# Kernel optimization log

Measured on AMD Instinct MI355X. Metric: run time of the kernel, lower is better.

Reference implementation:

```python
import jax, jax.numpy as jnp
import numpy as np


def setup_inputs() -> dict:
    key = jax.random.key(0)
    k1, k2 = jax.random.split(key)
    B, D, T = 8, 256, 4096
    Q, K = 8, 1024
    z = jax.random.normal(k1, (B, D, T), dtype=jnp.float32)
    # original init: uniform(-1/n_e, 1/n_e)
    codebooks = jax.random.uniform(k2, (Q, K, D), dtype=jnp.float32,
                                   minval=-1.0 / K, maxval=1.0 / K)
    return {"z": z, "codebooks": codebooks}


def reference(z, codebooks):
    # z: [B, e_dim, T]; codebooks: [Q, n_e, e_dim]
    zp = jnp.transpose(z, (0, 2, 1))  # [B, T, D]
    residual = zp
    quantized_out = jnp.zeros_like(zp)
    total_loss = jnp.zeros((), dtype=z.dtype)
    all_indices = []
    Q = codebooks.shape[0]
    for q in range(Q):  # small fixed number of residual stages
        E = codebooks[q]  # [K, D]
        # squared euclidean distances: ||r||^2 + ||e||^2 - 2 r.e
        d = (jnp.sum(residual ** 2, axis=-1, keepdims=True)
             + jnp.sum(E ** 2, axis=-1)
             - 2.0 * jnp.einsum('btd,kd->btk', residual, E))  # [B, T, K]
        idx = jnp.argmin(d, axis=-1)  # [B, T]
        z_q = E[idx]                  # [B, T, D] gather
        loss = (jnp.mean((jax.lax.stop_gradient(z_q) - residual) ** 2)
                + 0.25 * jnp.mean((z_q - jax.lax.stop_gradient(residual)) ** 2))
        # straight-through estimator
        z_q_st = residual + jax.lax.stop_gradient(z_q - residual)
        residual = residual - z_q_st
        quantized_out = quantized_out + z_q_st
        total_loss = total_loss + loss
        all_indices.append(idx)
    quantized_out = jnp.transpose(quantized_out, (0, 2, 1))  # [B, D, T]
    return quantized_out, total_loss, jnp.stack(all_indices)  # indices: [Q, B, T]
```

## Files before the change

### kernel.cpp

```cpp
#include <hip/hip_runtime.h>

#define B_   8
#define D_   256
#define T_   4096
#define Q_   8
#define K_   1024
#define BT_  (B_*T_)
#define N_   (B_*T_*D_)
#define LOSS_OFF N_
#define IDX_OFF  (N_+1)
#define ROWS 64
#define THREADS 1024

typedef __attribute__((ext_vector_type(8))) short short8;
typedef __attribute__((ext_vector_type(4))) float float4v;

union U4S8 { uint4 u; short8 s; };

__device__ __forceinline__ unsigned short f2bf(float x) {
    unsigned int u = __float_as_uint(x);
    unsigned int r = (u + 0x7FFFu + ((u >> 16) & 1u)) >> 16;
    return (unsigned short)r;
}
__device__ __forceinline__ float bf2f(unsigned short b) {
    return __uint_as_float(((unsigned int)b) << 16);
}
__device__ __forceinline__ unsigned fkey(float f) {
    unsigned u = __float_as_uint(f);
    return (u & 0x80000000u) ? ~u : (u | 0x80000000u);
}
__device__ __forceinline__ float fkeyinv(unsigned k) {
    unsigned u = (k & 0x80000000u) ? (k & 0x7fffffffu) : ~k;
    return __uint_as_float(u);
}


__global__ void k_init(const float* __restrict__ z, float* __restrict__ residual,
                       double* lossAcc) {
    __shared__ float tile[32][33];
    int b  = blockIdx.z;
    int d0 = blockIdx.y * 32;
    int t0 = blockIdx.x * 32;
    int tx = threadIdx.x & 31;
    int ty = threadIdx.x >> 5;
    const float* zb = z + (size_t)b * D_ * T_;
    #pragma unroll
    for (int r = 0; r < 32; r += 8)
        tile[ty + r][tx] = zb[(size_t)(d0 + ty + r) * T_ + t0 + tx];
    __syncthreads();
    float* rb = residual + (size_t)b * T_ * D_;
    #pragma unroll
    for (int r = 0; r < 32; r += 8)
        rb[(size_t)(t0 + ty + r) * D_ + d0 + tx] = tile[tx][ty + r];
    if (b == 0 && blockIdx.x == 0 && blockIdx.y == 0 && threadIdx.x == 0)
        *lossAcc = 0.0;
}


__global__ void k_bfrag(const float* __restrict__ cb, uint4* __restrict__ Bfrag) {
    int gid = blockIdx.x * 256 + threadIdx.x;
    int q    = gid >> 15;
    int rem  = gid & 32767;
    int ct   = rem >> 9;
    int kc   = (rem >> 6) & 7;
    int lane = rem & 63;
    int cand = ct * 16 + (lane & 15);
    int kb   = kc * 32 + (lane >> 4) * 8;
    const float* e = cb + ((size_t)q * K_ + cand) * D_ + kb;
    float4v u0 = *(const float4v*)(e);
    float4v u1 = *(const float4v*)(e + 4);
    float vv[8] = {u0.x, u0.y, u0.z, u0.w, u1.x, u1.y, u1.z, u1.w};
    unsigned short h[8], l[8];
    #pragma unroll
    for (int j = 0; j < 8; ++j) {
        float v = vv[j];
        h[j] = f2bf(v);
        l[j] = f2bf(v - bf2f(h[j]));
    }
    uint4 hi, lo;
    hi.x = (unsigned)h[0] | ((unsigned)h[1] << 16);
    hi.y = (unsigned)h[2] | ((unsigned)h[3] << 16);
    hi.z = (unsigned)h[4] | ((unsigned)h[5] << 16);
    hi.w = (unsigned)h[6] | ((unsigned)h[7] << 16);
    lo.x = (unsigned)l[0] | ((unsigned)l[1] << 16);
    lo.y = (unsigned)l[2] | ((unsigned)l[3] << 16);
    lo.z = (unsigned)l[4] | ((unsigned)l[5] << 16);
    lo.w = (unsigned)l[6] | ((unsigned)l[7] << 16);
    size_t base = (((size_t)(q * 64 + ct) * 8 + kc) * 2) * 64;
    Bfrag[base + lane]      = hi;
    Bfrag[base + 64 + lane] = lo;
}


__global__ void k_se(const float* __restrict__ cb, float* __restrict__ Se) {
    int gid = blockIdx.x * 256 + threadIdx.x;
    int i  = gid >> 4;
    int ln = gid & 15;
    if (i >= Q_ * K_) return;
    const float* e = cb + (size_t)i * D_ + ln * 16;
    float4v v0 = *(const float4v*)(e);
    float4v v1 = *(const float4v*)(e + 4);
    float4v v2 = *(const float4v*)(e + 8);
    float4v v3 = *(const float4v*)(e + 12);
    float vv[16] = {v0.x, v0.y, v0.z, v0.w, v1.x, v1.y, v1.z, v1.w,
                    v2.x, v2.y, v2.z, v2.w, v3.x, v3.y, v3.z, v3.w};
    double s = 0.0;
    #pragma unroll
    for (int d = 0; d < 16; ++d) {
        float a = vv[d] * vv[d];
        s += (double)a;
    }
    #pragma unroll
    for (int st = 8; st > 0; st >>= 1) s += __shfl_xor(s, st);
    if (ln == 0) Se[i] = (float)s;
}


__launch_bounds__(THREADS, 1)
__global__ void k_stage(const float* __restrict__ cb,
                        const uint4* __restrict__ Bfrag,
                        const float* __restrict__ Se,
                        float* __restrict__ residual,
                        float* __restrict__ out,
                        double* __restrict__ lossAcc,
                        int q) {
    __shared__ union {
        uint4 afr[4096];
        struct { int slist[64][16]; float sdd[64][16];
                 int srow[1024]; int sslot[1024]; } post;
        struct { float ovd[1024]; int ovk[1024]; } over;
        double lred[16];
    } sc;
    __shared__ float seL[1024];
    __shared__ float srb[64], margin[64];
    __shared__ unsigned sminI[64];
    __shared__ int   scount[64], sidx[64];
    __shared__ int   nSurv;

    const int tid  = threadIdx.x;
    const int lane = tid & 63;
    const int w    = tid >> 6;
    const int quad = lane >> 4;
    const int lc   = lane & 15;
    const int row0 = blockIdx.x * ROWS;
    const int g    = tid >> 8;
    const int dt   = tid & 255;

    if (tid < 64) { scount[tid] = 0; sminI[tid] = 0xFFFFFFFFu; }
    if (tid == 64) nSurv = 0;
    seL[tid] = Se[q * K_ + tid];

    const uint4* __restrict__ Bq = Bfrag + (size_t)q * (64 * 8 * 2 * 64);
    U4S8 bh0[2], bl0[2], bh1[2], bl1[2];
    #pragma unroll
    for (int c = 0; c < 2; ++c) {
        const uint4* p0 = Bq + (((size_t)((w * 4 + c) * 8 + 0)) * 2) * 64 + lane;
        bh0[c].u = p0[0]; bl0[c].u = p0[64];
        const uint4* p1 = Bq + (((size_t)((w * 4 + 2 + c) * 8 + 0)) * 2) * 64 + lane;
        bh1[c].u = p1[0]; bl1[c].u = p1[64];
    }

    {
        int row = tid >> 4, seg = tid & 15;
        int rg = row >> 4, rlo = row & 15;
        int kc = seg >> 1, par = seg & 1;
        const float* rp = residual + (size_t)(row0 + row) * D_ + seg * 16;
        float4v v0 = *(const float4v*)(rp);
        float4v v1 = *(const float4v*)(rp + 4);
        float4v v2 = *(const float4v*)(rp + 8);
        float4v v3 = *(const float4v*)(rp + 12);
        float vv[16] = {v0.x, v0.y, v0.z, v0.w, v1.x, v1.y, v1.z, v1.w,
                        v2.x, v2.y, v2.z, v2.w, v3.x, v3.y, v3.z, v3.w};
        double s = 0.0; float sa = 0.0f;
        #pragma unroll
        for (int i = 0; i < 16; ++i) {
            float v = vv[i];
            s += (double)(v * v);
            sa += fabsf(v);
        }
        #pragma unroll
        for (int st = 8; st > 0; st >>= 1) {
            s  += __shfl_xor(s, st);
            sa += __shfl_xor(sa, st);
        }
        if (seg == 0) {
            float sr = (float)s;
            float sb = sa * 1.001f;
            srb[row]    = sr;
            margin[row] = 9.6e-7f * sr + 4.0e-7f * sb + 2.0e-4f;
        }
        #pragma unroll
        for (int h = 0; h < 2; ++h) {
            unsigned short hh[8], ll[8];
            #pragma unroll
            for (int j = 0; j < 8; ++j) {
                float v = vv[h * 8 + j];
                hh[j] = f2bf(v);
                ll[j] = f2bf(v - bf2f(hh[j]));
            }
            uint4 hiW, loW;
            hiW.x = (unsigned)hh[0] | ((unsigned)hh[1] << 16);
            hiW.y = (unsigned)hh[2] | ((unsigned)hh[3] << 16);
            hiW.z = (unsigned)hh[4] | ((unsigned)hh[5] << 16);
            hiW.w = (unsigned)hh[6] | ((unsigned)hh[7] << 16);
            loW.x = (unsigned)ll[0] | ((unsigned)ll[1] << 16);
            loW.y = (unsigned)ll[2] | ((unsigned)ll[3] << 16);
            loW.z = (unsigned)ll[4] | ((unsigned)ll[5] << 16);
            loW.w = (unsigned)ll[6] | ((unsigned)ll[7] << 16);
            int ln = (par * 2 + h) * 16 + rlo;
            int sl = ln ^ kc;
            sc.afr[((rg * 8 + kc) * 2 + 0) * 64 + sl] = hiW;
            sc.afr[((rg * 8 + kc) * 2 + 1) * 64 + sl] = loW;
        }
    }
    __syncthreads();

    float4v accA[16];
    #pragma unroll
    for (int i = 0; i < 16; ++i) accA[i] = (float4v){0.f, 0.f, 0.f, 0.f};

    for (int s = 0; s < 16; ++s) {
        int kc = s >> 1;
        int cb0 = (s & 1) * 2;
        U4S8 bh[2], bl[2];
        if ((s & 1) == 0) { bh[0] = bh0[0]; bl[0] = bl0[0]; bh[1] = bh0[1]; bl[1] = bl0[1]; }
        else              { bh[0] = bh1[0]; bl[0] = bl1[0]; bh[1] = bh1[1]; bl[1] = bl1[1]; }
        {
            int ps  = (s + 2 > 15) ? 15 : (s + 2);
            int pkc = ps >> 1;
            int pc0 = (ps & 1) * 2;
            #pragma unroll
            for (int c = 0; c < 2; ++c) {
                const uint4* p = Bq + (((size_t)((w * 4 + pc0 + c) * 8 + pkc)) * 2) * 64 + lane;
                if ((s & 1) == 0) { bh0[c].u = p[0]; bl0[c].u = p[64]; }
                else              { bh1[c].u = p[0]; bl1[c].u = p[64]; }
            }
        }
        #pragma unroll
        for (int rg = 0; rg < 4; ++rg) {
            U4S8 ah, al;
            ah.u = sc.afr[((rg * 8 + kc) * 2 + 0) * 64 + (lane ^ kc)];
            al.u = sc.afr[((rg * 8 + kc) * 2 + 1) * 64 + (lane ^ kc)];
            #pragma unroll
            for (int c = 0; c < 2; ++c) {
                float4v a = accA[(cb0 + c) * 4 + rg];
                a = __builtin_amdgcn_mfma_f32_16x16x32_bf16(ah.s, bh[c].s, a, 0, 0, 0);
                a = __builtin_amdgcn_mfma_f32_16x16x32_bf16(al.s, bh[c].s, a, 0, 0, 0);
                a = __builtin_amdgcn_mfma_f32_16x16x32_bf16(ah.s, bl[c].s, a, 0, 0, 0);
                accA[(cb0 + c) * 4 + rg] = a;
            }
        }
    }

    float sr16[16];
    #pragma unroll
    for (int rr = 0; rr < 16; ++rr)
        sr16[rr] = srb[(rr >> 2) * 16 + quad * 4 + (rr & 3)];

    float mn[16];
    #pragma unroll
    for (int rr = 0; rr < 16; ++rr) mn[rr] = 3.4e38f;
    #pragma unroll
    for (int c = 0; c < 4; ++c) {
        int cand = (w * 4 + c) * 16 + lc;
        float se = seL[cand];
        #pragma unroll
        for (int rr = 0; rr < 16; ++rr) {
            float dd = (sr16[rr] + se) - 2.0f * accA[c * 4 + (rr >> 2)][rr & 3];
            mn[rr] = fminf(mn[rr], dd);
        }
    }
    #pragma unroll
    for (int rr = 0; rr < 16; ++rr) {
        float v = mn[rr];
        v = fminf(v, __shfl_xor(v, 1));
        v = fminf(v, __shfl_xor(v, 2));
        v = fminf(v, __shfl_xor(v, 4));
        v = fminf(v, __shfl_xor(v, 8));
        if (lc == 0)
            atomicMin(&sminI[(rr >> 2) * 16 + quad * 4 + (rr & 3)], fkey(v));
    }
    __syncthreads();

    #pragma unroll
    for (int c = 0; c < 4; ++c) {
        int cand = (w * 4 + c) * 16 + lc;
        float se = seL[cand];
        #pragma unroll
        for (int rr = 0; rr < 16; ++rr) {
            int row = (rr >> 2) * 16 + quad * 4 + (rr & 3);
            float dd = (sr16[rr] + se) - 2.0f * accA[c * 4 + (rr >> 2)][rr & 3];
            float thr = fkeyinv(sminI[row]) + margin[row];
            if (dd <= thr) {
                int p = atomicAdd(&scount[row], 1);
                if (p < 16) sc.post.slist[row][p] = cand;
            }
        }
    }
    __syncthreads();

    if (tid < 64) {
        int cnt = scount[tid];
        if (cnt == 1) {
            sidx[tid] = sc.post.slist[tid][0];
        } else if (cnt >= 2 && cnt <= 16) {
            int base = atomicAdd(&nSurv, cnt);
            for (int s2 = 0; s2 < cnt; ++s2) {
                sc.post.srow[base + s2]  = tid;
                sc.post.sslot[base + s2] = s2;
            }
        }
    }
    __syncthreads();

    {
        int nS  = nSurv;
        int grp = tid >> 4, ln = tid & 15;
        for (int j = grp; j < nS; j += 64) {
            int row  = sc.post.srow[j];
            int slot = sc.post.sslot[j];
            int k    = sc.post.slist[row][slot];
            const float* Ek = cb + ((size_t)q * K_ + k) * D_ + ln * 16;
            const float* Rk = residual + (size_t)(row0 + row) * D_ + ln * 16;
            float4v e0 = *(const float4v*)(Ek);
            float4v e1 = *(const float4v*)(Ek + 4);
            float4v e2 = *(const float4v*)(Ek + 8);
            float4v e3 = *(const float4v*)(Ek + 12);
            float4v r0 = *(const float4v*)(Rk);
            float4v r1 = *(const float4v*)(Rk + 4);
            float4v r2 = *(const float4v*)(Rk + 8);
            float4v r3 = *(const float4v*)(Rk + 12);
            float ev[16] = {e0.x, e0.y, e0.z, e0.w, e1.x, e1.y, e1.z, e1.w,
                            e2.x, e2.y, e2.z, e2.w, e3.x, e3.y, e3.z, e3.w};
            float rv2[16] = {r0.x, r0.y, r0.z, r0.w, r1.x, r1.y, r1.z, r1.w,
                             r2.x, r2.y, r2.z, r2.w, r3.x, r3.y, r3.z, r3.w};
            double a0 = 0.0, a1 = 0.0;
            #pragma unroll
            for (int d = 0; d < 16; d += 2) {
                a0 = fma((double)ev[d],     (double)rv2[d],     a0);
                a1 = fma((double)ev[d + 1], (double)rv2[d + 1], a1);
            }
            double ssum = a0 + a1;
            #pragma unroll
            for (int st = 8; st > 0; st >>= 1) ssum += __shfl_xor(ssum, st);
            if (ln == 0) {
                float dotf = (float)ssum;
                float V = srb[row] + seL[k];
                sc.post.sdd[row][slot] = V - 2.0f * dotf;
            }
        }
    }
    __syncthreads();
    if (tid < 64) {
        int cnt = scount[tid];
        if (cnt >= 2 && cnt <= 16) {
            float bd = 3.4e38f; int bk = 0x7fffffff;
            for (int s2 = 0; s2 < cnt; ++s2) {
                float dv = sc.post.sdd[tid][s2]; int kv = sc.post.slist[tid][s2];
                if (dv < bd || (dv == bd && kv < bk)) { bd = dv; bk = kv; }
            }
            sidx[tid] = bk;
        }
    }
    __syncthreads();

    for (int row = 0; row < ROWS; ++row) {
        int cnt = scount[row];
        if (cnt <= 16) continue;
        const float* Rr = residual + (size_t)(row0 + row) * D_;
        int k = tid;
        const float* Ek = cb + ((size_t)q * K_ + k) * D_;
        double a0 = 0.0, a1 = 0.0;
        for (int d = 0; d < D_; d += 2) {
            a0 = fma((double)Ek[d],     (double)Rr[d],     a0);
            a1 = fma((double)Ek[d + 1], (double)Rr[d + 1], a1);
        }
        float bd = (srb[row] + seL[k]) - 2.0f * (float)(a0 + a1);
        sc.over.ovd[tid] = bd; sc.over.ovk[tid] = k;
        __syncthreads();
        for (int st = 512; st > 0; st >>= 1) {
            if (tid < st) {
                float od = sc.over.ovd[tid + st]; int ok = sc.over.ovk[tid + st];
                if (od < sc.over.ovd[tid] ||
                    (od == sc.over.ovd[tid] && ok < sc.over.ovk[tid])) {
                    sc.over.ovd[tid] = od; sc.over.ovk[tid] = ok;
                }
            }
            __syncthreads();
        }
        if (tid == 0) sidx[row] = sc.over.ovk[0];
        __syncthreads();
    }

    const float* Eq = cb + (size_t)q * K_ * D_;
    double lsum = 0.0;
    #pragma unroll
    for (int jj = 0; jj < 16; ++jj) {
        int row = g * 16 + jj;
        int idx = sidx[row];
        size_t roff = (size_t)(row0 + row) * D_ + dt;
        float rv   = residual[roff];
        float zq   = Eq[(size_t)idx * D_ + dt];
        float t1   = zq - rv;
        float zqst = rv + t1;
        residual[roff] = rv - zqst;
        lsum += (double)t1 * (double)t1;
    }
    if (tid < 64) out[IDX_OFF + q * BT_ + row0 + tid] = (float)sidx[tid];

    #pragma unroll
    for (int st = 32; st > 0; st >>= 1) lsum += __shfl_xor(lsum, st);
    __syncthreads();
    if (lane == 0) sc.lred[w] = lsum;
    __syncthreads();
    if (tid == 0) {
        double t = 0.0;
        #pragma unroll
        for (int i = 0; i < 16; ++i) t += sc.lred[i];
        atomicAdd(lossAcc, t);
    }
}


__global__ void k_emit(const float* __restrict__ z, const float* __restrict__ residual,
                       float* __restrict__ out) {
    __shared__ float tile[32][33];
    int b  = blockIdx.z;
    int t0 = blockIdx.y * 32;
    int d0 = blockIdx.x * 32;
    int tx = threadIdx.x & 31;
    int ty = threadIdx.x >> 5;
    const float* rb = residual + (size_t)b * T_ * D_;
    #pragma unroll
    for (int r = 0; r < 32; r += 8)
        tile[ty + r][tx] = rb[(size_t)(t0 + ty + r) * D_ + d0 + tx];
    __syncthreads();
    const float* zb = z + (size_t)b * D_ * T_;
    float* ob = out + (size_t)b * D_ * T_;
    #pragma unroll
    for (int r = 0; r < 32; r += 8) {
        size_t off = (size_t)(d0 + ty + r) * T_ + t0 + tx;
        ob[off] = zb[off] - tile[tx][ty + r];
    }
}

__global__ void k_final(const double* lossAcc, float* out) {
    if (threadIdx.x == 0 && blockIdx.x == 0) {
        double m = *lossAcc / (double)N_;
        out[LOSS_OFF] = (float)(1.25 * m);
    }
}


extern "C" void kernel_launch(void* const* d_in, const int* in_sizes, int n_in,
                              void* d_out, int out_size, void* d_ws, size_t ws_size,
                              hipStream_t stream) {
    const float* z  = (const float*)d_in[0];
    const float* cb = (const float*)d_in[1];
    float* out = (float*)d_out;

    float*  residual = (float*)d_ws;
    uint4*  Bfrag    = (uint4*)((char*)d_ws + (size_t)N_ * 4);
    float*  Se       = (float*)((char*)d_ws + (size_t)N_ * 4 + (size_t)8 * 1024 * 1024);
    double* lossAcc  = (double*)((char*)d_ws + (size_t)N_ * 4 + (size_t)8 * 1024 * 1024
                                 + (size_t)Q_ * K_ * 4);

    hipLaunchKernelGGL(k_init, dim3(T_ / 32, D_ / 32, B_), dim3(256), 0, stream,
                       z, residual, lossAcc);
    hipLaunchKernelGGL(k_bfrag, dim3(1024), dim3(256), 0, stream, cb, Bfrag);
    hipLaunchKernelGGL(k_se, dim3((Q_ * K_ * 16 + 255) / 256), dim3(256), 0, stream,
                       cb, Se);
    for (int q = 0; q < Q_; ++q) {
        hipLaunchKernelGGL(k_stage, dim3(BT_ / ROWS), dim3(THREADS), 0, stream,
                           cb, Bfrag, Se, residual, out, lossAcc, q);
    }
    hipLaunchKernelGGL(k_emit, dim3(D_ / 32, T_ / 32, B_), dim3(256), 0, stream,
                       z, residual, out);
    hipLaunchKernelGGL(k_final, dim3(1), dim3(256), 0, stream, lossAcc, out);
}
```

Baseline: 781.1 us.

## Restructure MFMA loop to per-kc A fragments, single-tile B prefetch, enforce 4 waves/EU

The main GEMM loop now iterates over 8 k-chunks, loads all four row-group A fragments from shared memory once per chunk, and streams B tiles one at a time through a two-deep register prefetch ring. This replaces the earlier two-pairs-at-a-time double buffer. The launch bounds drop the min-blocks hint and add amdgpu_waves_per_eu(4,4) to pin the register budget. The shared A buffer also grows from 4096 to 5120 entries, which raises LDS use and may reduce occupancy. The goal is to cut B register pressure and redundant LDS A loads, at the risk of less latency hiding per prefetch.

```diff
diff --git a/kernel.cpp b/kernel.cpp
--- a/kernel.cpp
+++ b/kernel.cpp
@@ -116,16 +116,17 @@
 }
 
 
-__launch_bounds__(THREADS, 1)
-__global__ void k_stage(const float* __restrict__ cb,
-                        const uint4* __restrict__ Bfrag,
-                        const float* __restrict__ Se,
-                        float* __restrict__ residual,
-                        float* __restrict__ out,
-                        double* __restrict__ lossAcc,
-                        int q) {
+__global__ void __launch_bounds__(THREADS)
+__attribute__((amdgpu_waves_per_eu(4, 4)))
+k_stage(const float* __restrict__ cb,
+        const uint4* __restrict__ Bfrag,
+        const float* __restrict__ Se,
+        float* __restrict__ residual,
+        float* __restrict__ out,
+        double* __restrict__ lossAcc,
+        int q) {
     __shared__ union {
-        uint4 afr[4096];
+        uint4 afr[5120];
         struct { int slist[64][16]; float sdd[64][16];
                  int srow[1024]; int sslot[1024]; } post;
         struct { float ovd[1024]; int ovk[1024]; } over;
@@ -151,13 +152,11 @@
     seL[tid] = Se[q * K_ + tid];
 
     const uint4* __restrict__ Bq = Bfrag + (size_t)q * (64 * 8 * 2 * 64);
-    U4S8 bh0[2], bl0[2], bh1[2], bl1[2];
-    #pragma unroll
-    for (int c = 0; c < 2; ++c) {
-        const uint4* p0 = Bq + (((size_t)((w * 4 + c) * 8 + 0)) * 2) * 64 + lane;
-        bh0[c].u = p0[0]; bl0[c].u = p0[64];
-        const uint4* p1 = Bq + (((size_t)((w * 4 + 2 + c) * 8 + 0)) * 2) * 64 + lane;
-        bh1[c].u = p1[0]; bl1[c].u = p1[64];
+    U4S8 bufh[2], bufl[2];
+    #pragma unroll
+    for (int t = 0; t < 2; ++t) {
+        const uint4* p = Bq + (((size_t)((w * 4 + (t & 3)) * 8 + (t >> 2))) * 2) * 64 + lane;
+        bufh[t].u = p[0]; bufl[t].u = p[64];
     }
 
     {
@@ -219,35 +218,29 @@
     #pragma unroll
     for (int i = 0; i < 16; ++i) accA[i] = (float4v){0.f, 0.f, 0.f, 0.f};
 
-    for (int s = 0; s < 16; ++s) {
-        int kc = s >> 1;
-        int cb0 = (s & 1) * 2;
-        U4S8 bh[2], bl[2];
-        if ((s & 1) == 0) { bh[0] = bh0[0]; bl[0] = bl0[0]; bh[1] = bh0[1]; bl[1] = bl0[1]; }
-        else              { bh[0] = bh1[0]; bl[0] = bl1[0]; bh[1] = bh1[1]; bl[1] = bl1[1]; }
-        {
-            int ps  = (s + 2 > 15) ? 15 : (s + 2);
-            int pkc = ps >> 1;
-            int pc0 = (ps & 1) * 2;
+    for (int kc = 0; kc < 8; ++kc) {
+        U4S8 ah[4], al[4];
+        #pragma unroll
+        for (int rg = 0; rg < 4; ++rg) {
+            ah[rg].u = sc.afr[((rg * 8 + kc) * 2 + 0) * 64 + (lane ^ kc)];
+            al[rg].u = sc.afr[((rg * 8 + kc) * 2 + 1) * 64 + (lane ^ kc)];
+        }
+        #pragma unroll
+        for (int c = 0; c < 4; ++c) {
+            int t = kc * 4 + c;
+            U4S8 bh = bufh[t & 1], bl = bufl[t & 1];
+            {
+                int pt = (t + 2 > 31) ? 31 : (t + 2);
+                const uint4* p = Bq + (((size_t)((w * 4 + (pt & 3)) * 8 + (pt >> 2))) * 2) * 64 + lane;
+                bufh[t & 1].u = p[0]; bufl[t & 1].u = p[64];
+            }
             #pragma unroll
-            for (int c = 0; c < 2; ++c) {
-                const uint4* p = Bq + (((size_t)((w * 4 + pc0 + c) * 8 + pkc)) * 2) * 64 + lane;
-                if ((s & 1) == 0) { bh0[c].u = p[0]; bl0[c].u = p[64]; }
-                else              { bh1[c].u = p[0]; bl1[c].u = p[64]; }
-            }
-        }
-        #pragma unroll
-        for (int rg = 0; rg < 4; ++rg) {
-            U4S8 ah, al;
-            ah.u = sc.afr[((rg * 8 + kc) * 2 + 0) * 64 + (lane ^ kc)];
-            al.u = sc.afr[((rg * 8 + kc) * 2 + 1) * 64 + (lane ^ kc)];
-            #pragma unroll
-            for (int c = 0; c < 2; ++c) {
-                float4v a = accA[(cb0 + c) * 4 + rg];
-                a = __builtin_amdgcn_mfma_f32_16x16x32_bf16(ah.s, bh[c].s, a, 0, 0, 0);
-                a = __builtin_amdgcn_mfma_f32_16x16x32_bf16(al.s, bh[c].s, a, 0, 0, 0);
-                a = __builtin_amdgcn_mfma_f32_16x16x32_bf16(ah.s, bl[c].s, a, 0, 0, 0);
-                accA[(cb0 + c) * 4 + rg] = a;
+            for (int rg = 0; rg < 4; ++rg) {
+                float4v a = accA[c * 4 + rg];
+                a = __builtin_amdgcn_mfma_f32_16x16x32_bf16(ah[rg].s, bh.s, a, 0, 0, 0);
+                a = __builtin_amdgcn_mfma_f32_16x16x32_bf16(al[rg].s, bh.s, a, 0, 0, 0);
+                a = __builtin_amdgcn_mfma_f32_16x16x32_bf16(ah[rg].s, bl.s, a, 0, 0, 0);
+                accA[c * 4 + rg] = a;
             }
         }
     }
```

New measurement: 903.5 us. 1.16x slower.
